# Optimization experiments

Hardware: AMD Instinct MI355X
Metric: run time of the kernel (lower is better)

## Reference

```python
import jax, jax.numpy as jnp
import numpy as np

B, C, H, W = 64, 64, 56, 56
MID = 2 * C  # two output nodes concatenated
EPS = 1e-5


def _conv1x1(x, w):
    # x: [B,C,H,W], w: [O,C] (1x1 conv kernel squeezed)
    return jnp.einsum('bchw,oc->bohw', x, w)


def _bn(x, g, b, m, v):
    # eval-mode BatchNorm2d with running stats
    sc = g * jax.lax.rsqrt(v + EPS)
    return x * sc[None, :, None, None] + (b - m * sc)[None, :, None, None]


def _maxpool3(x):
    # MaxPool2d(kernel=3, stride=1, padding=1)
    return jax.lax.reduce_window(x, -jnp.inf, jax.lax.max,
                                 (1, 1, 3, 3), (1, 1, 1, 1),
                                 [(0, 0), (0, 0), (1, 1), (1, 1)])


def _avgpool3(x):
    # AvgPool2d(kernel=3, stride=1, padding=1), count_include_pad=True -> /9
    s = jax.lax.reduce_window(x, 0.0, jax.lax.add,
                              (1, 1, 3, 3), (1, 1, 1, 1),
                              [(0, 0), (0, 0), (1, 1), (1, 1)])
    return s * (1.0 / 9.0)


def setup_inputs() -> dict:
    key = jax.random.key(0)
    ks = jax.random.split(key, 11)
    x = jax.random.normal(ks[0], (B, C, H, W), dtype=jnp.float32)
    w1 = jax.random.normal(ks[1], (C, C), dtype=jnp.float32) * 0.1
    w2 = jax.random.normal(ks[2], (C, MID), dtype=jnp.float32) * 0.1
    bn1_g = 1.0 + 0.1 * jax.random.normal(ks[3], (C,), dtype=jnp.float32)
    bn1_b = 0.1 * jax.random.normal(ks[4], (C,), dtype=jnp.float32)
    bn1_m = 0.1 * jax.random.normal(ks[5], (C,), dtype=jnp.float32)
    bn1_v = jax.random.uniform(ks[6], (C,), minval=0.5, maxval=1.5, dtype=jnp.float32)
    bn2_g = 1.0 + 0.1 * jax.random.normal(ks[7], (C,), dtype=jnp.float32)
    bn2_b = 0.1 * jax.random.normal(ks[8], (C,), dtype=jnp.float32)
    bn2_m = 0.1 * jax.random.normal(ks[9], (C,), dtype=jnp.float32)
    bn2_v = jax.random.uniform(ks[10], (C,), minval=0.5, maxval=1.5, dtype=jnp.float32)
    return dict(x=x, w1=w1, w2=w2,
                bn1_g=bn1_g, bn1_b=bn1_b, bn1_m=bn1_m, bn1_v=bn1_v,
                bn2_g=bn2_g, bn2_b=bn2_b, bn2_m=bn2_m, bn2_v=bn2_v)


def reference(x, w1, w2, bn1_g, bn1_b, bn1_m, bn1_v, bn2_g, bn2_b, bn2_m, bn2_v):
    # DAG g = [[[0,1],[1,2]], [[4,3],[3]], [[5,3],[3,100]], [[4,3],[100]]]
    # topoSort order: [0, 2, 1, 3]; output nodes (ordered): [2, 3]
    node0 = jax.nn.relu(_bn(_conv1x1(x, w1), bn1_g, bn1_b, bn1_m, bn1_v))
    node1 = _maxpool3(node0)            # op type 4, pred {0}
    node2 = _avgpool3(node0)            # op type 5, pred {0}
    node3 = _maxpool3(node1) + _maxpool3(node2)  # op type 4, preds {1,2}, summed
    cat = jnp.concatenate([node2, node3], axis=1)  # [B, 2C, H, W]
    out = jax.nn.relu(_bn(_conv1x1(cat, w2), bn2_g, bn2_b, bn2_m, bn2_v))
    return out
```

## Files before the change

kernel.cpp:

```cpp
#include <hip/hip_runtime.h>
#include <cstddef>

#define EPS 1e-5f
static constexpr int Bn = 64, Cn = 64, Hn = 56, Wn = 56, HWn = Hn * Wn;
static constexpr int RB = 8;
static constexpr int NBAND = 7;
static constexpr int SLAB = 3600;

typedef __attribute__((ext_vector_type(8))) short short8;
typedef __attribute__((ext_vector_type(8))) unsigned short ushort8;
typedef __attribute__((ext_vector_type(4))) unsigned short ushort4v;
typedef __attribute__((ext_vector_type(4))) float floatx4;
typedef __attribute__((ext_vector_type(16))) float floatx16;
typedef __attribute__((ext_vector_type(4))) unsigned int uintx4;
typedef __attribute__((ext_vector_type(2))) unsigned int uintx2;

__device__ __forceinline__ unsigned pack_rne(float a, float b) {
    unsigned ua = __float_as_uint(a), ub = __float_as_uint(b);
    ua = ua + 0x7fffu + ((ua >> 16) & 1u);
    ub = ub + 0x7fffu + ((ub >> 16) & 1u);
    return __builtin_amdgcn_perm(ub, ua, 0x07060302);
}
__device__ __forceinline__ unsigned pack_trunc(float a, float b) {
    return __builtin_amdgcn_perm(__float_as_uint(b), __float_as_uint(a), 0x07060302);
}
__device__ __forceinline__ uintx2 pmax2(uintx2 a, uintx2 b) {
    ushort4v r = __builtin_elementwise_max(*(ushort4v*)&a, *(ushort4v*)&b);
    return *(uintx2*)&r;
}
__device__ __forceinline__ float bf_lo(unsigned u) { return __uint_as_float(u << 16); }
__device__ __forceinline__ float bf_hi(unsigned u) { return __uint_as_float(u & 0xffff0000u); }


__global__ __launch_bounds__(256, 4) void k1_conv1(
    const float* __restrict__ x, const float* __restrict__ w1,
    const float* __restrict__ bg, const float* __restrict__ bb,
    const float* __restrict__ bm, const float* __restrict__ bv,
    unsigned short* __restrict__ node0)
{
    __shared__ float scs[64], shs[64];
    const int tid = threadIdx.x;
    if (tid < 64) {
        float sc = bg[tid] * rsqrtf(bv[tid] + EPS);
        scs[tid] = sc;
        shs[tid] = bb[tid] - bm[tid] * sc;
    }
    __syncthreads();
    const int lane = tid & 63;
    const int wv   = tid >> 6;
    const int n    = lane & 31;
    const int h    = lane >> 5;

    short8 afr0[4], afr1[4];
    {
        const float s0 = scs[n], s1 = scs[32 + n];
        #pragma unroll
        for (int kt = 0; kt < 4; ++kt) {
            const float* wp0 = w1 + (size_t)n * 64 + kt * 16 + h * 8;
            floatx4 f0 = *(const floatx4*)wp0;
            floatx4 f1 = *(const floatx4*)(wp0 + 4);
            uintx4 u;
            u.x = pack_rne(f0[0] * s0, f0[1] * s0);
            u.y = pack_rne(f0[2] * s0, f0[3] * s0);
            u.z = pack_rne(f1[0] * s0, f1[1] * s0);
            u.w = pack_rne(f1[2] * s0, f1[3] * s0);
            afr0[kt] = *(short8*)&u;
            const float* wp1 = wp0 + 32 * 64;
            floatx4 g0 = *(const floatx4*)wp1;
            floatx4 g1 = *(const floatx4*)(wp1 + 4);
            uintx4 v;
            v.x = pack_rne(g0[0] * s1, g0[1] * s1);
            v.y = pack_rne(g0[2] * s1, g0[3] * s1);
            v.z = pack_rne(g1[0] * s1, g1[1] * s1);
            v.w = pack_rne(g1[2] * s1, g1[3] * s1);
            afr1[kt] = *(short8*)&v;
        }
    }

    #pragma unroll
    for (int s = 0; s < 2; ++s) {
        const int P = blockIdx.x * 256 + (wv * 2 + s) * 32;
        const int b = P / HWn, p0 = P - b * HWn;
        const float* xb = x + (size_t)b * 64 * HWn + p0 + n;

        float f[4][8];
        #pragma unroll
        for (int kt = 0; kt < 4; ++kt)
            #pragma unroll
            for (int j = 0; j < 8; ++j)
                f[kt][j] = xb[(size_t)(kt * 16 + h * 8 + j) * HWn];

        floatx16 acc0, acc1;
        #pragma unroll
        for (int i = 0; i < 16; ++i) { acc0[i] = 0.f; acc1[i] = 0.f; }

        #pragma unroll
        for (int kt = 0; kt < 4; ++kt) {
            uintx4 u;
            u.x = pack_trunc(f[kt][0], f[kt][1]);
            u.y = pack_trunc(f[kt][2], f[kt][3]);
            u.z = pack_trunc(f[kt][4], f[kt][5]);
            u.w = pack_trunc(f[kt][6], f[kt][7]);
            short8 bfr = *(short8*)&u;
            acc0 = __builtin_amdgcn_mfma_f32_32x32x16_bf16(afr0[kt], bfr, acc0, 0, 0, 0);
            acc1 = __builtin_amdgcn_mfma_f32_32x32x16_bf16(afr1[kt], bfr, acc1, 0, 0, 0);
        }

        #pragma unroll
        for (int oct = 0; oct < 2; ++oct) {
            #pragma unroll
            for (int g = 0; g < 4; ++g) {
                floatx4 sh4 = *(const floatx4*)&shs[oct * 32 + g * 8 + h * 4];
                float v0 = (oct ? acc1[g * 4 + 0] : acc0[g * 4 + 0]) + sh4[0]; v0 = v0 > 0.f ? v0 : 0.f;
                float v1 = (oct ? acc1[g * 4 + 1] : acc0[g * 4 + 1]) + sh4[1]; v1 = v1 > 0.f ? v1 : 0.f;
                float v2 = (oct ? acc1[g * 4 + 2] : acc0[g * 4 + 2]) + sh4[2]; v2 = v2 > 0.f ? v2 : 0.f;
                float v3 = (oct ? acc1[g * 4 + 3] : acc0[g * 4 + 3]) + sh4[3]; v3 = v3 > 0.f ? v3 : 0.f;
                uintx2 st;
                st.x = pack_rne(v0, v1);
                st.y = pack_rne(v2, v3);
                const int chunk = oct * 4 + g;
                *(uintx2*)(node0 + ((size_t)(b * 8 + chunk) * HWn + p0 + n) * 8 + h * 4) = st;
            }
        }
    }
}

__global__ __launch_bounds__(1024, 4) void k23_fused(
    const unsigned short* __restrict__ node0,
    const float* __restrict__ w2,
    const float* __restrict__ bg, const float* __restrict__ bb,
    const float* __restrict__ bm, const float* __restrict__ bv,
    float* __restrict__ out)
{
    __shared__ __align__(16) unsigned short catl[16 * SLAB];
    const int tid = threadIdx.x;
    const int lane = tid & 63;
    const int wv = tid >> 6;

    const int bid = blockIdx.x;
    const int xcd = bid & 7;
    const int jj = bid >> 3;
    const int b = xcd * 8 + jj / NBAND;
    const int band = jj % NBAND;
    const int lo = band * RB;

    {
        const int chunk = wv >> 1;
        const int c0 = (wv & 1) * 28;
        const int local = lane >> 1;
        const int col = c0 - 2 + local;
        const int jh = lane & 1;
        const unsigned short* base = node0 + ((size_t)(b * 8 + chunk) * HWn) * 8 + jh * 4;

        const uintx2 zz = (uintx2){0u, 0u};
        auto loadrow = [&](int r) -> uintx2 {
            if (((unsigned)col >= (unsigned)Wn) | ((unsigned)r >= (unsigned)Hn)) return zz;
            return *(const uintx2*)(base + (size_t)(r * Wn + col) * 8);
        };

        float hs1[4], hs2[4];
        #pragma unroll
        for (int c = 0; c < 4; ++c) hs1[c] = hs2[c] = 0.f;
        uintx2 h5a = zz, h5b = zz, h5c = zz, h5d = zz, nh1 = zz, nh2 = zz;

        uintx2 cur = loadrow(lo - 2);
        uintx2 nxt = loadrow(lo - 1);

        unsigned short* cav = catl + (size_t)(chunk * 2) * SLAB + jh * 4;
        unsigned short* cmx = cav + SLAB;
        const bool stcol = (local >= 2) & (local <= 29);

        #pragma unroll
        for (int i = 0; i < RB + 4; ++i) {
            const int r = lo - 2 + i;
            uintx2 nx2 = (i < RB + 2) ? loadrow(r + 2) : zz;

            uintx2 D0, D1, D3, D4;
            #pragma unroll
            for (int w = 0; w < 2; ++w) {
                unsigned u = cur[w];
                D1[w] = __shfl_up(u, 2);
                D0[w] = __shfl_up(u, 4);
                D3[w] = __shfl_down(u, 2);
                D4[w] = __shfl_down(u, 4);
            }

            uintx2 hm5 = pmax2(pmax2(pmax2(D0, D1), pmax2(cur, D3)), D4);
            uintx2 m5 = pmax2(pmax2(pmax2(h5a, h5b), pmax2(h5c, h5d)), hm5);
            h5a = h5b; h5b = h5c; h5c = h5d; h5d = hm5;

            float a2[4];
            #pragma unroll
            for (int w = 0; w < 2; ++w) {
                float s0 = bf_lo(D1[w]) + bf_lo(cur[w]) + bf_lo(D3[w]);
                float s1 = bf_hi(D1[w]) + bf_hi(cur[w]) + bf_hi(D3[w]);
                a2[w * 2 + 0] = (hs2[w * 2 + 0] + hs1[w * 2 + 0] + s0) * (1.f / 9.f);
                a2[w * 2 + 1] = (hs2[w * 2 + 1] + hs1[w * 2 + 1] + s1) * (1.f / 9.f);
                hs2[w * 2 + 0] = hs1[w * 2 + 0]; hs1[w * 2 + 0] = s0;
                hs2[w * 2 + 1] = hs1[w * 2 + 1]; hs1[w * 2 + 1] = s1;
            }
            uintx2 ap;
            ap.x = pack_rne(a2[0], a2[1]);
            ap.y = pack_rne(a2[2], a2[3]);

            uintx2 al, ar;
            #pragma unroll
            for (int w = 0; w < 2; ++w) {
                al[w] = __shfl_up(ap[w], 2);
                ar[w] = __shfl_down(ap[w], 2);
            }
            uintx2 nh = pmax2(pmax2(al, ap), ar);
            uintx2 m3 = pmax2(pmax2(nh2, nh1), nh);
            nh2 = nh1; nh1 = nh;

            const int r2 = r - 1, r3 = r - 2;
            if (stcol && i >= 3 && i <= RB + 2)
                *(uintx2*)(cav + (size_t)((r2 - lo) * Wn + col) * 8) = ap;
            if (stcol && i >= 4) {
                uintx2 st;
                st.x = pack_rne(bf_lo(m5.x) + bf_lo(m3.x), bf_hi(m5.x) + bf_hi(m3.x));
                st.y = pack_rne(bf_lo(m5.y) + bf_lo(m3.y), bf_hi(m5.y) + bf_hi(m3.y));
                *(uintx2*)(cmx + (size_t)((r3 - lo) * Wn + col) * 8) = st;
            }
            cur = nxt; nxt = nx2;
        }
    }

    const int m16 = lane & 15;
    const int q = lane >> 4;
    const int t = wv & 3;
    const int e = wv >> 2;
    short8 afr[4];
    #pragma unroll
    for (int cp = 0; cp < 4; ++cp) {
        const int c = 2 * cp + (q >> 1);
        const int chb = ((q & 1) ? 64 : 0) + 8 * c;
        const float* wp = w2 + (size_t)(t * 16 + m16) * 128 + chb;
        floatx4 f0 = *(const floatx4*)wp;
        floatx4 f1 = *(const floatx4*)(wp + 4);
        uintx4 u;
        u.x = pack_rne(f0[0], f0[1]);
        u.y = pack_rne(f0[2], f0[3]);
        u.z = pack_rne(f1[0], f1[1]);
        u.w = pack_rne(f1[2], f1[3]);
        afr[cp] = *(short8*)&u;
    }
    const int oc0 = t * 16 + q * 4;
    floatx4 g4 = *(const floatx4*)(bg + oc0);
    floatx4 bb4 = *(const floatx4*)(bb + oc0);
    floatx4 mm4 = *(const floatx4*)(bm + oc0);
    floatx4 vv4 = *(const floatx4*)(bv + oc0);
    float sc[4], sh[4];
    #pragma unroll
    for (int r = 0; r < 4; ++r) {
        sc[r] = g4[r] * rsqrtf(vv4[r] + EPS);
        sh[r] = bb4[r] - mm4[r] * sc[r];
    }
    __syncthreads();

    floatx4 acc[7];
    #pragma unroll
    for (int i = 0; i < 7; ++i) acc[i] = (floatx4){0.f, 0.f, 0.f, 0.f};

    #pragma unroll
    for (int cp = 0; cp < 4; ++cp) {
        #pragma unroll
        for (int i = 0; i < 7; ++i) {
            const int px = (e * 7 + i) * 16 + m16;
            short8 bfr = *(const short8*)(catl + (size_t)(4 * cp + q) * SLAB + (size_t)px * 8);
            acc[i] = __builtin_amdgcn_mfma_f32_16x16x32_bf16(afr[cp], bfr, acc[i], 0, 0, 0);
        }
    }

    float* ob = out + (size_t)(b * 64 + oc0) * HWn + lo * Wn;
    #pragma unroll
    for (int i = 0; i < 7; ++i) {
        const int px = (e * 7 + i) * 16 + m16;
        #pragma unroll
        for (int r = 0; r < 4; ++r) {
            float v = fmaf(acc[i][r], sc[r], sh[r]);
            ob[(size_t)r * HWn + px] = v > 0.f ? v : 0.f;
        }
    }
}

extern "C" void kernel_launch(void* const* d_in, const int* in_sizes, int n_in,
                              void* d_out, int out_size, void* d_ws, size_t ws_size,
                              hipStream_t stream)
{
    const float* x   = (const float*)d_in[0];
    const float* w1  = (const float*)d_in[1];
    const float* w2  = (const float*)d_in[2];
    const float* b1g = (const float*)d_in[3];
    const float* b1b = (const float*)d_in[4];
    const float* b1m = (const float*)d_in[5];
    const float* b1v = (const float*)d_in[6];
    const float* b2g = (const float*)d_in[7];
    const float* b2b = (const float*)d_in[8];
    const float* b2m = (const float*)d_in[9];
    const float* b2v = (const float*)d_in[10];

    float* out = (float*)d_out;
    unsigned short* node0 = (unsigned short*)d_ws;

    k1_conv1<<<dim3(784), dim3(256), 0, stream>>>(x, w1, b1g, b1b, b1m, b1v, node0);
    k23_fused<<<dim3(Bn * NBAND), dim3(1024), 0, stream>>>(node0, w2, b2g, b2b, b2m, b2v, out);
}
```

Measured before the change: 148.2 us.

## Fuse conv1 into pooling/conv2 kernel with per-band halo recompute in LDS

Merges the two kernels into one. Each block recomputes the first 1x1 conv plus BN and ReLU for its 7-row band and a 2-row halo on each side, and keeps node0 in LDS instead of writing it to global workspace and reading it back. The pooling and second conv stage now runs in two passes per band so the cat buffer fits in the smaller LDS slab. This removes the node0 global round trip and one launch, at the cost of recomputing halo rows (11 computed for every 7 kept), heavy LDS use that limits occupancy, and extra barriers.

```diff
diff --git a/kernel.cpp b/kernel.cpp
--- a/kernel.cpp
+++ b/kernel.cpp
@@ -3,12 +3,13 @@
 
 #define EPS 1e-5f
 static constexpr int Bn = 64, Cn = 64, Hn = 56, Wn = 56, HWn = Hn * Wn;
-static constexpr int RB = 8;
-static constexpr int NBAND = 7;
-static constexpr int SLAB = 3600;
+static constexpr int RB = 7;
+static constexpr int NBAND = 8;
+static constexpr int TROWS = 11;
+static constexpr int CHS = TROWS * Wn * 8;
+static constexpr int SLAB = 1808;
 
 typedef __attribute__((ext_vector_type(8))) short short8;
-typedef __attribute__((ext_vector_type(8))) unsigned short ushort8;
 typedef __attribute__((ext_vector_type(4))) unsigned short ushort4v;
 typedef __attribute__((ext_vector_type(4))) float floatx4;
 typedef __attribute__((ext_vector_type(16))) float floatx16;
@@ -32,27 +33,42 @@
 __device__ __forceinline__ float bf_hi(unsigned u) { return __uint_as_float(u & 0xffff0000u); }
 
 
-__global__ __launch_bounds__(256, 4) void k1_conv1(
+__global__ __launch_bounds__(1024) void k_fused(
     const float* __restrict__ x, const float* __restrict__ w1,
-    const float* __restrict__ bg, const float* __restrict__ bb,
-    const float* __restrict__ bm, const float* __restrict__ bv,
-    unsigned short* __restrict__ node0)
+    const float* __restrict__ w2,
+    const float* __restrict__ b1g, const float* __restrict__ b1b,
+    const float* __restrict__ b1m, const float* __restrict__ b1v,
+    const float* __restrict__ b2g, const float* __restrict__ b2b,
+    const float* __restrict__ b2m, const float* __restrict__ b2v,
+    float* __restrict__ out)
 {
-    __shared__ float scs[64], shs[64];
+    __shared__ __align__(16) unsigned short n0l[8 * CHS];
+    __shared__ __align__(16) unsigned short catl[16 * SLAB];
+    __shared__ __align__(16) float scs[64], shs[64];
+
     const int tid = threadIdx.x;
+    const int lane = tid & 63;
+    const int wv = tid >> 6;
+
     if (tid < 64) {
-        float sc = bg[tid] * rsqrtf(bv[tid] + EPS);
+        float sc = b1g[tid] * rsqrtf(b1v[tid] + EPS);
         scs[tid] = sc;
-        shs[tid] = bb[tid] - bm[tid] * sc;
-    }
+        shs[tid] = b1b[tid] - b1m[tid] * sc;
+    }
+
+    const int bid = blockIdx.x;
+    const int xcd = bid & 7;
+    const int jj = bid >> 3;
+    const int b = xcd * 8 + (jj >> 3);
+    const int band = jj & 7;
+    const int lo = band * RB;
+
     __syncthreads();
-    const int lane = tid & 63;
-    const int wv   = tid >> 6;
-    const int n    = lane & 31;
-    const int h    = lane >> 5;
-
-    short8 afr0[4], afr1[4];
+
+    const int n = lane & 31;
+    const int h = lane >> 5;
     {
+        short8 afr0[4], afr1[4];
         const float s0 = scs[n], s1 = scs[32 + n];
         #pragma unroll
         for (int kt = 0; kt < 4; ++kt) {
@@ -75,154 +91,58 @@
             v.w = pack_rne(g1[2] * s1, g1[3] * s1);
             afr1[kt] = *(short8*)&v;
         }
-    }
-
-    #pragma unroll
-    for (int s = 0; s < 2; ++s) {
-        const int P = blockIdx.x * 256 + (wv * 2 + s) * 32;
-        const int b = P / HWn, p0 = P - b * HWn;
-        const float* xb = x + (size_t)b * 64 * HWn + p0 + n;
-
-        float f[4][8];
-        #pragma unroll
-        for (int kt = 0; kt < 4; ++kt)
-            #pragma unroll
-            for (int j = 0; j < 8; ++j)
-                f[kt][j] = xb[(size_t)(kt * 16 + h * 8 + j) * HWn];
-
-        floatx16 acc0, acc1;
-        #pragma unroll
-        for (int i = 0; i < 16; ++i) { acc0[i] = 0.f; acc1[i] = 0.f; }
-
-        #pragma unroll
-        for (int kt = 0; kt < 4; ++kt) {
-            uintx4 u;
-            u.x = pack_trunc(f[kt][0], f[kt][1]);
-            u.y = pack_trunc(f[kt][2], f[kt][3]);
-            u.z = pack_trunc(f[kt][4], f[kt][5]);
-            u.w = pack_trunc(f[kt][6], f[kt][7]);
-            short8 bfr = *(short8*)&u;
-            acc0 = __builtin_amdgcn_mfma_f32_32x32x16_bf16(afr0[kt], bfr, acc0, 0, 0, 0);
-            acc1 = __builtin_amdgcn_mfma_f32_32x32x16_bf16(afr1[kt], bfr, acc1, 0, 0, 0);
-        }
-
-        #pragma unroll
-        for (int oct = 0; oct < 2; ++oct) {
-            #pragma unroll
-            for (int g = 0; g < 4; ++g) {
-                floatx4 sh4 = *(const floatx4*)&shs[oct * 32 + g * 8 + h * 4];
-                float v0 = (oct ? acc1[g * 4 + 0] : acc0[g * 4 + 0]) + sh4[0]; v0 = v0 > 0.f ? v0 : 0.f;
-                float v1 = (oct ? acc1[g * 4 + 1] : acc0[g * 4 + 1]) + sh4[1]; v1 = v1 > 0.f ? v1 : 0.f;
-                float v2 = (oct ? acc1[g * 4 + 2] : acc0[g * 4 + 2]) + sh4[2]; v2 = v2 > 0.f ? v2 : 0.f;
-                float v3 = (oct ? acc1[g * 4 + 3] : acc0[g * 4 + 3]) + sh4[3]; v3 = v3 > 0.f ? v3 : 0.f;
-                uintx2 st;
-                st.x = pack_rne(v0, v1);
-                st.y = pack_rne(v2, v3);
-                const int chunk = oct * 4 + g;
-                *(uintx2*)(node0 + ((size_t)(b * 8 + chunk) * HWn + p0 + n) * 8 + h * 4) = st;
-            }
-        }
-    }
-}
-
-__global__ __launch_bounds__(1024, 4) void k23_fused(
-    const unsigned short* __restrict__ node0,
-    const float* __restrict__ w2,
-    const float* __restrict__ bg, const float* __restrict__ bb,
-    const float* __restrict__ bm, const float* __restrict__ bv,
-    float* __restrict__ out)
-{
-    __shared__ __align__(16) unsigned short catl[16 * SLAB];
-    const int tid = threadIdx.x;
-    const int lane = tid & 63;
-    const int wv = tid >> 6;
-
-    const int bid = blockIdx.x;
-    const int xcd = bid & 7;
-    const int jj = bid >> 3;
-    const int b = xcd * 8 + jj / NBAND;
-    const int band = jj % NBAND;
-    const int lo = band * RB;
-
-    {
-        const int chunk = wv >> 1;
-        const int c0 = (wv & 1) * 28;
-        const int local = lane >> 1;
-        const int col = c0 - 2 + local;
-        const int jh = lane & 1;
-        const unsigned short* base = node0 + ((size_t)(b * 8 + chunk) * HWn) * 8 + jh * 4;
-
-        const uintx2 zz = (uintx2){0u, 0u};
-        auto loadrow = [&](int r) -> uintx2 {
-            if (((unsigned)col >= (unsigned)Wn) | ((unsigned)r >= (unsigned)Hn)) return zz;
-            return *(const uintx2*)(base + (size_t)(r * Wn + col) * 8);
-        };
-
-        float hs1[4], hs2[4];
-        #pragma unroll
-        for (int c = 0; c < 4; ++c) hs1[c] = hs2[c] = 0.f;
-        uintx2 h5a = zz, h5b = zz, h5c = zz, h5d = zz, nh1 = zz, nh2 = zz;
-
-        uintx2 cur = loadrow(lo - 2);
-        uintx2 nxt = loadrow(lo - 1);
-
-        unsigned short* cav = catl + (size_t)(chunk * 2) * SLAB + jh * 4;
-        unsigned short* cmx = cav + SLAB;
-        const bool stcol = (local >= 2) & (local <= 29);
-
-        #pragma unroll
-        for (int i = 0; i < RB + 4; ++i) {
-            const int r = lo - 2 + i;
-            uintx2 nx2 = (i < RB + 2) ? loadrow(r + 2) : zz;
-
-            uintx2 D0, D1, D3, D4;
-            #pragma unroll
-            for (int w = 0; w < 2; ++w) {
-                unsigned u = cur[w];
-                D1[w] = __shfl_up(u, 2);
-                D0[w] = __shfl_up(u, 4);
-                D3[w] = __shfl_down(u, 2);
-                D4[w] = __shfl_down(u, 4);
-            }
-
-            uintx2 hm5 = pmax2(pmax2(pmax2(D0, D1), pmax2(cur, D3)), D4);
-            uintx2 m5 = pmax2(pmax2(pmax2(h5a, h5b), pmax2(h5c, h5d)), hm5);
-            h5a = h5b; h5b = h5c; h5c = h5d; h5d = hm5;
-
-            float a2[4];
-            #pragma unroll
-            for (int w = 0; w < 2; ++w) {
-                float s0 = bf_lo(D1[w]) + bf_lo(cur[w]) + bf_lo(D3[w]);
-                float s1 = bf_hi(D1[w]) + bf_hi(cur[w]) + bf_hi(D3[w]);
-                a2[w * 2 + 0] = (hs2[w * 2 + 0] + hs1[w * 2 + 0] + s0) * (1.f / 9.f);
-                a2[w * 2 + 1] = (hs2[w * 2 + 1] + hs1[w * 2 + 1] + s1) * (1.f / 9.f);
-                hs2[w * 2 + 0] = hs1[w * 2 + 0]; hs1[w * 2 + 0] = s0;
-                hs2[w * 2 + 1] = hs1[w * 2 + 1]; hs1[w * 2 + 1] = s1;
-            }
-            uintx2 ap;
-            ap.x = pack_rne(a2[0], a2[1]);
-            ap.y = pack_rne(a2[2], a2[3]);
-
-            uintx2 al, ar;
-            #pragma unroll
-            for (int w = 0; w < 2; ++w) {
-                al[w] = __shfl_up(ap[w], 2);
-                ar[w] = __shfl_down(ap[w], 2);
-            }
-            uintx2 nh = pmax2(pmax2(al, ap), ar);
-            uintx2 m3 = pmax2(pmax2(nh2, nh1), nh);
-            nh2 = nh1; nh1 = nh;
-
-            const int r2 = r - 1, r3 = r - 2;
-            if (stcol && i >= 3 && i <= RB + 2)
-                *(uintx2*)(cav + (size_t)((r2 - lo) * Wn + col) * 8) = ap;
-            if (stcol && i >= 4) {
-                uintx2 st;
-                st.x = pack_rne(bf_lo(m5.x) + bf_lo(m3.x), bf_hi(m5.x) + bf_hi(m3.x));
-                st.y = pack_rne(bf_lo(m5.y) + bf_lo(m3.y), bf_hi(m5.y) + bf_hi(m3.y));
-                *(uintx2*)(cmx + (size_t)((r3 - lo) * Wn + col) * 8) = st;
-            }
-            cur = nxt; nxt = nx2;
+
+        const int r0 = (lo - 2 < 0) ? 0 : lo - 2;
+        const int r1 = (lo + RB + 2 > Hn) ? Hn : lo + RB + 2;
+        const int npx = (r1 - r0) * Wn;
+        const int nt = (npx + 31) >> 5;
+        const int rowoff = r0 - (lo - 2);
+        const float* xb = x + (size_t)b * 64 * HWn + r0 * Wn;
+
+        for (int ti = wv; ti < nt; ti += 16) {
+            const int p0 = ti * 32;
+            const int gi = (p0 + n < npx) ? (p0 + n) : (npx - 1);
+            float f[4][8];
+            #pragma unroll
+            for (int kt = 0; kt < 4; ++kt)
+                #pragma unroll
+                for (int j = 0; j < 8; ++j)
+                    f[kt][j] = xb[(size_t)(kt * 16 + h * 8 + j) * HWn + gi];
+
+            floatx16 acc0, acc1;
+            #pragma unroll
+            for (int i = 0; i < 16; ++i) { acc0[i] = 0.f; acc1[i] = 0.f; }
+
+            #pragma unroll
+            for (int kt = 0; kt < 4; ++kt) {
+                uintx4 u;
+                u.x = pack_trunc(f[kt][0], f[kt][1]);
+                u.y = pack_trunc(f[kt][2], f[kt][3]);
+                u.z = pack_trunc(f[kt][4], f[kt][5]);
+                u.w = pack_trunc(f[kt][6], f[kt][7]);
+                short8 bfr = *(short8*)&u;
+                acc0 = __builtin_amdgcn_mfma_f32_32x32x16_bf16(afr0[kt], bfr, acc0, 0, 0, 0);
+                acc1 = __builtin_amdgcn_mfma_f32_32x32x16_bf16(afr1[kt], bfr, acc1, 0, 0, 0);
+            }
+
+            const bool stok = (p0 + n) < npx;
+            unsigned short* np0 = n0l + (size_t)(rowoff * Wn + p0 + n) * 8 + h * 4;
+            #pragma unroll
+            for (int oct = 0; oct < 2; ++oct) {
+                #pragma unroll
+                for (int g = 0; g < 4; ++g) {
+                    floatx4 sh4 = *(const floatx4*)&shs[oct * 32 + g * 8 + h * 4];
+                    float v0 = (oct ? acc1[g * 4 + 0] : acc0[g * 4 + 0]) + sh4[0]; v0 = v0 > 0.f ? v0 : 0.f;
+                    float v1 = (oct ? acc1[g * 4 + 1] : acc0[g * 4 + 1]) + sh4[1]; v1 = v1 > 0.f ? v1 : 0.f;
+                    float v2 = (oct ? acc1[g * 4 + 2] : acc0[g * 4 + 2]) + sh4[2]; v2 = v2 > 0.f ? v2 : 0.f;
+                    float v3 = (oct ? acc1[g * 4 + 3] : acc0[g * 4 + 3]) + sh4[3]; v3 = v3 > 0.f ? v3 : 0.f;
+                    uintx2 st;
+                    st.x = pack_rne(v0, v1);
+                    st.y = pack_rne(v2, v3);
+                    if (stok)
+                        *(uintx2*)(np0 + (size_t)(oct * 4 + g) * CHS) = st;
+                }
+            }
         }
     }
 
@@ -246,41 +166,120 @@
         afr[cp] = *(short8*)&u;
     }
     const int oc0 = t * 16 + q * 4;
-    floatx4 g4 = *(const floatx4*)(bg + oc0);
-    floatx4 bb4 = *(const floatx4*)(bb + oc0);
-    floatx4 mm4 = *(const floatx4*)(bm + oc0);
-    floatx4 vv4 = *(const floatx4*)(bv + oc0);
-    float sc[4], sh[4];
+    floatx4 g4 = *(const floatx4*)(b2g + oc0);
+    floatx4 bb4 = *(const floatx4*)(b2b + oc0);
+    floatx4 mm4 = *(const floatx4*)(b2m + oc0);
+    floatx4 vv4 = *(const floatx4*)(b2v + oc0);
+    float sc2[4], sh2[4];
     #pragma unroll
     for (int r = 0; r < 4; ++r) {
-        sc[r] = g4[r] * rsqrtf(vv4[r] + EPS);
-        sh[r] = bb4[r] - mm4[r] * sc[r];
+        sc2[r] = g4[r] * rsqrtf(vv4[r] + EPS);
+        sh2[r] = bb4[r] - mm4[r] * sc2[r];
     }
     __syncthreads();
 
-    floatx4 acc[7];
-    #pragma unroll
-    for (int i = 0; i < 7; ++i) acc[i] = (floatx4){0.f, 0.f, 0.f, 0.f};
-
-    #pragma unroll
-    for (int cp = 0; cp < 4; ++cp) {
-        #pragma unroll
-        for (int i = 0; i < 7; ++i) {
-            const int px = (e * 7 + i) * 16 + m16;
-            short8 bfr = *(const short8*)(catl + (size_t)(4 * cp + q) * SLAB + (size_t)px * 8);
-            acc[i] = __builtin_amdgcn_mfma_f32_16x16x32_bf16(afr[cp], bfr, acc[i], 0, 0, 0);
+    const int chunk = wv >> 1;
+    const int c0 = (wv & 1) * 28;
+    const int local = lane >> 1;
+    const int col = c0 - 2 + local;
+    const int jh = lane & 1;
+    const bool colok = (unsigned)col < (unsigned)Wn;
+    const bool stcol = (local >= 2) & (local <= 29);
+    const unsigned short* nb = n0l + (size_t)chunk * CHS + jh * 4;
+    unsigned short* cav = catl + (size_t)(chunk * 2) * SLAB + jh * 4;
+    unsigned short* cmx = cav + SLAB;
+    const uintx2 zz = (uintx2){0u, 0u};
+
+    float* ob = out + (size_t)(b * 64 + oc0) * HWn;
+
+    for (int p = 0; p < 2; ++p) {
+        const int lop = lo + 4 * p;
+        const int nr = p ? (RB - 4) : 4;
+
+        {
+            float hs1[4], hs2[4];
+            #pragma unroll
+            for (int c = 0; c < 4; ++c) hs1[c] = hs2[c] = 0.f;
+            uintx2 h5a = zz, h5b = zz, h5c = zz, h5d = zz, nh1 = zz, nh2 = zz;
+
+            for (int i = 0; i < nr + 4; ++i) {
+                const int r = lop - 2 + i;
+                uintx2 cur = zz;
+                if (colok & ((unsigned)r < (unsigned)Hn))
+                    cur = *(const uintx2*)(nb + (size_t)((r - lo + 2) * Wn + col) * 8);
+
+                uintx2 D0, D1, D3, D4;
+                #pragma unroll
+                for (int w = 0; w < 2; ++w) {
+                    unsigned u = cur[w];
+                    D1[w] = __shfl_up(u, 2);
+                    D0[w] = __shfl_up(u, 4);
+                    D3[w] = __shfl_down(u, 2);
+                    D4[w] = __shfl_down(u, 4);
+                }
+
+                uintx2 hm5 = pmax2(pmax2(pmax2(D0, D1), pmax2(cur, D3)), D4);
+                uintx2 m5 = pmax2(pmax2(pmax2(h5a, h5b), pmax2(h5c, h5d)), hm5);
+                h5a = h5b; h5b = h5c; h5c = h5d; h5d = hm5;
+
+                float a2[4];
+                #pragma unroll
+                for (int w = 0; w < 2; ++w) {
+                    float s0 = bf_lo(D1[w]) + bf_lo(cur[w]) + bf_lo(D3[w]);
+                    float s1 = bf_hi(D1[w]) + bf_hi(cur[w]) + bf_hi(D3[w]);
+                    a2[w * 2 + 0] = (hs2[w * 2 + 0] + hs1[w * 2 + 0] + s0) * (1.f / 9.f);
+                    a2[w * 2 + 1] = (hs2[w * 2 + 1] + hs1[w * 2 + 1] + s1) * (1.f / 9.f);
+                    hs2[w * 2 + 0] = hs1[w * 2 + 0]; hs1[w * 2 + 0] = s0;
+                    hs2[w * 2 + 1] = hs1[w * 2 + 1]; hs1[w * 2 + 1] = s1;
+                }
+                uintx2 ap;
+                ap.x = pack_rne(a2[0], a2[1]);
+                ap.y = pack_rne(a2[2], a2[3]);
+
+                uintx2 al, ar;
+                #pragma unroll
+                for (int w = 0; w < 2; ++w) {
+                    al[w] = __shfl_up(ap[w], 2);
+                    ar[w] = __shfl_down(ap[w], 2);
+                }
+                uintx2 nh = pmax2(pmax2(al, ap), ar);
+                uintx2 m3 = pmax2(pmax2(nh2, nh1), nh);
+                nh2 = nh1; nh1 = nh;
+
+                const int r2 = r - 1, r3 = r - 2;
+                if (stcol && i >= 3 && i <= nr + 2)
+                    *(uintx2*)(cav + (size_t)((r2 - lop) * Wn + col) * 8) = ap;
+                if (stcol && i >= 4) {
+                    uintx2 st;
+                    st.x = pack_rne(bf_lo(m5.x) + bf_lo(m3.x), bf_hi(m5.x) + bf_hi(m3.x));
+                    st.y = pack_rne(bf_lo(m5.y) + bf_lo(m3.y), bf_hi(m5.y) + bf_hi(m3.y));
+                    *(uintx2*)(cmx + (size_t)((r3 - lop) * Wn + col) * 8) = st;
+                }
+            }
         }
-    }
-
-    float* ob = out + (size_t)(b * 64 + oc0) * HWn + lo * Wn;
-    #pragma unroll
-    for (int i = 0; i < 7; ++i) {
-        const int px = (e * 7 + i) * 16 + m16;
-        #pragma unroll
-        for (int r = 0; r < 4; ++r) {
-            float v = fmaf(acc[i][r], sc[r], sh[r]);
-            ob[(size_t)r * HWn + px] = v > 0.f ? v : 0.f;
+        __syncthreads();
+
+        const int npxc = nr * Wn;
+        const int nPT = (npxc + 15) >> 4;
+        for (int k = 0; k < 4; ++k) {
+            const int pt = e + 4 * k;
+            if (pt >= nPT) break;
+            const int px = pt * 16 + m16;
+            floatx4 acc = (floatx4){0.f, 0.f, 0.f, 0.f};
+            #pragma unroll
+            for (int cp = 0; cp < 4; ++cp) {
+                short8 bfr = *(const short8*)(catl + (size_t)(4 * cp + q) * SLAB + (size_t)px * 8);
+                acc = __builtin_amdgcn_mfma_f32_16x16x32_bf16(afr[cp], bfr, acc, 0, 0, 0);
+            }
+            if (px < npxc) {
+                #pragma unroll
+                for (int r = 0; r < 4; ++r) {
+                    float v = fmaf(acc[r], sc2[r], sh2[r]);
+                    ob[(size_t)r * HWn + lop * Wn + px] = v > 0.f ? v : 0.f;
+                }
+            }
         }
+        __syncthreads();
     }
 }
 
@@ -301,8 +300,8 @@
     const float* b2v = (const float*)d_in[10];
 
     float* out = (float*)d_out;
-    unsigned short* node0 = (unsigned short*)d_ws;
-
-    k1_conv1<<<dim3(784), dim3(256), 0, stream>>>(x, w1, b1g, b1b, b1m, b1v, node0);
-    k23_fused<<<dim3(Bn * NBAND), dim3(1024), 0, stream>>>(node0, w2, b2g, b2b, b2m, b2v, out);
-}
+    (void)d_ws; (void)ws_size;
+
+    k_fused<<<dim3(Bn * NBAND), dim3(1024), 0, stream>>>(
+        x, w1, w2, b1g, b1b, b1m, b1v, b2g, b2b, b2m, b2v, out);
+}
```

After: 166.5 us. +12.3%, slower.
